# Kernel tuning notes

Hardware: AMD Instinct MI355X
Metric: run time of the kernel (lower is better)

The kernel has to match this reference:

```python
import jax, jax.numpy as jnp
import numpy as np

DIM = 2048
HEADS = 16
DIM_HEAD = 128
DIM_INNER = HEADS * DIM_HEAD  # 2048
EPS = 1.1920929e-07  # torch RMSNorm default eps = finfo(float32).eps


def setup_inputs() -> dict:
    key = jax.random.key(0)
    k_tok, k_q, k_kv, k_o = jax.random.split(key, 4)
    tokens = jax.random.normal(k_tok, (4, 2048, DIM), dtype=jnp.float32)
    # Linear weights stored as [in, out]; torch init ~ U(-1/sqrt(in), 1/sqrt(in)), use scaled normal
    s = 0.02
    w_q = jax.random.normal(k_q, (DIM, DIM_INNER), dtype=jnp.float32) * s
    w_kv = jax.random.normal(k_kv, (DIM, 2 * DIM_INNER), dtype=jnp.float32) * s
    w_out = jax.random.normal(k_o, (DIM_INNER, DIM), dtype=jnp.float32) * s
    norm_weight = jnp.ones((DIM,), dtype=jnp.float32)
    return {"tokens": tokens, "norm_weight": norm_weight, "w_q": w_q, "w_kv": w_kv, "w_out": w_out}


def _rmsnorm(x, weight):
    var = jnp.mean(jnp.square(x), axis=-1, keepdims=True)
    return x * jax.lax.rsqrt(var + EPS) * weight


def reference(tokens, norm_weight, w_q, w_kv, w_out):
    b, n, _ = tokens.shape
    x = _rmsnorm(tokens, norm_weight)
    q = x @ w_q                       # [b, n, h*d]
    kv = x @ w_kv                     # [b, n, 2*h*d]
    k, v = jnp.split(kv, 2, axis=-1)

    def split_heads(t):
        return t.reshape(b, n, HEADS, DIM_HEAD).transpose(0, 2, 1, 3)  # b h n d

    q, k, v = map(split_heads, (q, k, v))
    q = q * (DIM_HEAD ** -0.5)
    sim = jnp.einsum('bhid,bhjd->bhij', q, k)
    attn = jax.nn.softmax(sim, axis=-1)
    out = jnp.einsum('bhij,bhjd->bhid', attn, v)
    out = out.transpose(0, 2, 1, 3).reshape(b, n, DIM_INNER)
    return out @ w_out
```

## Files before the change

kernel.cpp:

```cpp
#include <hip/hip_runtime.h>
#include <hip/hip_bf16.h>
#include <stdint.h>

#define SEQ   2048
#define DIM   2048
#define HEADS 16
#define DHEAD 128
#define BATCH 4
#define MROWS (BATCH*SEQ)

typedef short bf16x8 __attribute__((ext_vector_type(8)));
typedef float f32x4  __attribute__((ext_vector_type(4)));
typedef float f32x16 __attribute__((ext_vector_type(16)));
typedef unsigned short u16x8 __attribute__((ext_vector_type(8)));
typedef unsigned int u32x4 __attribute__((ext_vector_type(4)));

__device__ __forceinline__ short f2bf(float f){
  union { float fv; unsigned u; } x; x.fv = f;
  unsigned r = x.u + 0x7fffu + ((x.u >> 16) & 1u);
  return (short)(r >> 16);
}

__device__ __forceinline__ unsigned cvtpk(float lo, float hi){
  unsigned r; asm("v_cvt_pk_bf16_f32 %0, %1, %2" : "=v"(r) : "v"(lo), "v"(hi)); return r;
}

__device__ __forceinline__ float exp2a(float x){
#if __has_builtin(__builtin_amdgcn_exp2f)
  return __builtin_amdgcn_exp2f(x);
#else
  return exp2f(x);
#endif
}

__device__ __forceinline__ void gl_lds16(const void* g, void* l){
  __builtin_amdgcn_global_load_lds((const __attribute__((address_space(1))) void*)g,
                                   (__attribute__((address_space(3))) void*)l, 16, 0, 0);
}

__device__ __forceinline__ void ofence(){
  asm volatile("" ::: "memory");
  __builtin_amdgcn_sched_barrier(0);
}

__global__ __launch_bounds__(256) void rmsnorm_cast_k(const float* __restrict__ tok,
                                                      const float* __restrict__ w,
                                                      short* __restrict__ x){
  const int row = blockIdx.x;
  const float4* r4 = (const float4*)(tok + (size_t)row * DIM);
  float4 a = r4[threadIdx.x * 2];
  float4 b = r4[threadIdx.x * 2 + 1];
  float ss = a.x*a.x + a.y*a.y + a.z*a.z + a.w*a.w
           + b.x*b.x + b.y*b.y + b.z*b.z + b.w*b.w;
  #pragma unroll
  for (int m = 1; m < 64; m <<= 1) ss += __shfl_xor(ss, m, 64);
  __shared__ float red[4];
  if ((threadIdx.x & 63) == 0) red[threadIdx.x >> 6] = ss;
  __syncthreads();
  float tot = red[0] + red[1] + red[2] + red[3];
  float rs = rsqrtf(tot * (1.0f / DIM) + 1.1920929e-07f);
  const float4* w4 = (const float4*)w;
  float4 wa = w4[threadIdx.x * 2];
  float4 wb = w4[threadIdx.x * 2 + 1];
  u16x8 o;
  o[0] = (unsigned short)f2bf(a.x * rs * wa.x);
  o[1] = (unsigned short)f2bf(a.y * rs * wa.y);
  o[2] = (unsigned short)f2bf(a.z * rs * wa.z);
  o[3] = (unsigned short)f2bf(a.w * rs * wa.w);
  o[4] = (unsigned short)f2bf(b.x * rs * wb.x);
  o[5] = (unsigned short)f2bf(b.y * rs * wb.y);
  o[6] = (unsigned short)f2bf(b.z * rs * wb.z);
  o[7] = (unsigned short)f2bf(b.w * rs * wb.w);
  *(u16x8*)(x + (size_t)row * DIM + threadIdx.x * 8) = o;
}

__global__ __launch_bounds__(256) void wtrans_k(const float* __restrict__ w,
                                                short* __restrict__ wt,
                                                int K, int N){
  __shared__ float tile[64][65];
  const int r0 = blockIdx.y * 64;
  const int c0 = blockIdx.x * 64;
  const int t = threadIdx.x;
  #pragma unroll
  for (int i = 0; i < 16; i++){
    int e = i * 256 + t; int r = e >> 6, c = e & 63;
    tile[r][c] = w[(size_t)(r0 + r) * N + c0 + c];
  }
  __syncthreads();
  #pragma unroll
  for (int i = 0; i < 16; i++){
    int e = i * 256 + t; int c = e >> 6, r = e & 63;
    wt[(size_t)(c0 + c) * K + r0 + r] = f2bf(tile[r][c]);
  }
}

__global__ __launch_bounds__(256) void vtrans_k(const short* __restrict__ kv,
                                                short* __restrict__ vt){
  __shared__ short tile[64][65];
  const int n0 = blockIdx.x * 64;
  const int d0 = blockIdx.y * 64;
  const int bh = blockIdx.z;
  const int b = bh >> 4, h = bh & 15;
  const int t = threadIdx.x;
  #pragma unroll
  for (int i = 0; i < 16; i++){
    int e = i * 256 + t; int r = e >> 6, c = e & 63;
    tile[r][c] = kv[(size_t)(b * SEQ + n0 + r) * 4096 + 2048 + h * DHEAD + d0 + c];
  }
  __syncthreads();
  #pragma unroll
  for (int i = 0; i < 16; i++){
    int e = i * 256 + t; int c = e >> 6, r = e & 63;
    vt[(size_t)(bh * DHEAD + d0 + c) * SEQ + n0 + r] = tile[r][c];
  }
}

__device__ __forceinline__ void storeC(float* C, size_t idx, float v){ C[idx] = v; }
__device__ __forceinline__ void storeC(short* C, size_t idx, float v){ C[idx] = f2bf(v); }

template<typename OutT>
__global__ __launch_bounds__(512, 2) void gemm256_k(const short* __restrict__ A,
                                                    const short* __restrict__ Bt,
                                                    OutT* __restrict__ C,
                                                    int M, int N, int K, int lgntn){
  __shared__ __align__(16) short As[4][256 * 32];
  __shared__ __align__(16) short Bs[4][256 * 32];
  const int nwg = gridDim.x;
  const int bid = blockIdx.x;
  const int o = (bid & 7) * (nwg >> 3) + (bid >> 3);
  const int bm = o >> lgntn, bn = o & ((1 << lgntn) - 1);
  const int m0 = bm << 8, n0 = bn << 8;
  const int tid = threadIdx.x, lane = tid & 63, wid = tid >> 6;
  const int l31 = lane & 31, hi = lane >> 5;
  const int wr = wid >> 2, wc = wid & 3;
  const int NT = K >> 5;

  f32x16 acc[4][2] = {};

  auto stageA = [&](int t){
    const int slot = t & 3;
    const size_t kbase = (size_t)t << 5;
    #pragma unroll
    for (int i = 0; i < 2; i++){
      int c = i * 512 + tid;
      int row = c >> 2;
      int j = (c & 3) ^ ((row >> 1) & 3);
      gl_lds16(A + (size_t)(m0 + row) * K + kbase + j * 8,
               &As[slot][(i * 512 + wid * 64) * 8]);
    }
  };
  auto stageB = [&](int t){
    const int slot = t & 3;
    const size_t kbase = (size_t)t << 5;
    #pragma unroll
    for (int i = 0; i < 2; i++){
      int c = i * 512 + tid;
      int row = c >> 2;
      int j = (c & 3) ^ ((row >> 1) & 3);
      gl_lds16(Bt + (size_t)(n0 + row) * K + kbase + j * 8,
               &Bs[slot][(i * 512 + wid * 64) * 8]);
    }
  };

  stageA(0); stageB(0); ofence();
  stageA(1); stageB(1); ofence();
  stageA(2); stageB(2); ofence();
  asm volatile("s_waitcnt vmcnt(8)" ::: "memory");
  __builtin_amdgcn_s_barrier();

  for (int t = 0; t < NT; t++){
    const short* Ab = As[t & 3];
    const short* Bb = Bs[t & 3];

    bf16x8 bfv[2][2], af0[2][2];
    #pragma unroll
    for (int nb = 0; nb < 2; nb++){
      int row = wc * 64 + nb * 32 + l31;
      #pragma unroll
      for (int ks = 0; ks < 2; ks++){
        int ch = (ks * 2 + hi) ^ ((row >> 1) & 3);
        bfv[nb][ks] = *(const bf16x8*)&Bb[row * 32 + ch * 8];
      }
    }
    #pragma unroll
    for (int mb = 0; mb < 2; mb++){
      int row = wr * 128 + mb * 32 + l31;
      #pragma unroll
      for (int ks = 0; ks < 2; ks++){
        int ch = (ks * 2 + hi) ^ ((row >> 1) & 3);
        af0[mb][ks] = *(const bf16x8*)&Ab[row * 32 + ch * 8];
      }
    }
    if (t + 3 < NT){ stageA(t + 3); ofence(); }
    __builtin_amdgcn_s_barrier();
    __builtin_amdgcn_s_setprio(1);
    #pragma unroll
    for (int mb = 0; mb < 2; mb++)
      #pragma unroll
      for (int nb = 0; nb < 2; nb++)
        #pragma unroll
        for (int ks = 0; ks < 2; ks++)
          acc[mb][nb] = __builtin_amdgcn_mfma_f32_32x32x16_bf16(af0[mb][ks], bfv[nb][ks],
                                                               acc[mb][nb], 0, 0, 0);
    __builtin_amdgcn_s_setprio(0);

    bf16x8 af1[2][2];
    #pragma unroll
    for (int mb = 0; mb < 2; mb++){
      int row = wr * 128 + (mb + 2) * 32 + l31;
      #pragma unroll
      for (int ks = 0; ks < 2; ks++){
        int ch = (ks * 2 + hi) ^ ((row >> 1) & 3);
        af1[mb][ks] = *(const bf16x8*)&Ab[row * 32 + ch * 8];
      }
    }
    if (t + 3 < NT){ stageB(t + 3); ofence(); }
    __builtin_amdgcn_s_barrier();
    __builtin_amdgcn_s_setprio(1);
    #pragma unroll
    for (int mb = 0; mb < 2; mb++)
      #pragma unroll
      for (int nb = 0; nb < 2; nb++)
        #pragma unroll
        for (int ks = 0; ks < 2; ks++)
          acc[mb + 2][nb] = __builtin_amdgcn_mfma_f32_32x32x16_bf16(af1[mb][ks], bfv[nb][ks],
                                                                   acc[mb + 2][nb], 0, 0, 0);
    __builtin_amdgcn_s_setprio(0);

    if (t + 1 < NT){
      if (t + 3 < NT)      asm volatile("s_waitcnt vmcnt(8)" ::: "memory");
      else if (t + 2 < NT) asm volatile("s_waitcnt vmcnt(4)" ::: "memory");
      else                 asm volatile("s_waitcnt vmcnt(0)" ::: "memory");
      __builtin_amdgcn_s_barrier();
    }
  }

  #pragma unroll
  for (int mb = 0; mb < 4; mb++)
    #pragma unroll
    for (int nb = 0; nb < 2; nb++)
      #pragma unroll
      for (int reg = 0; reg < 16; reg++){
        int r = (reg & 3) + 8 * (reg >> 2) + 4 * hi;
        int row = m0 + wr * 128 + mb * 32 + r;
        int col = n0 + wc * 64 + nb * 32 + l31;
        storeC(C, (size_t)row * N + col, acc[mb][nb][reg]);
      }
}

__global__ __launch_bounds__(256) void attn_k(const short* __restrict__ q,
                                              const short* __restrict__ kv,
                                              const short* __restrict__ vt,
                                              short* __restrict__ out){
  __shared__ __align__(16) short Ks[2][64 * 128];
  __shared__ __align__(16) short Vts[2][128 * 64];
  const int qt = blockIdx.x, bh = blockIdx.y;
  const int b = bh >> 4, h = bh & 15;
  const int tid = threadIdx.x, lane = tid & 63, wid = tid >> 6;
  const int l31 = lane & 31, hi = lane >> 5;
  const int qrow0 = qt * 128 + wid * 32;
  const float c2 = 0.08838834764831845f * 1.4426950408889634f;
  const int NT = SEQ / 64;

  bf16x8 qf[8];
  {
    const short* qp = q + (size_t)(b * SEQ + qrow0 + l31) * DIM + h * DHEAD + hi * 8;
    #pragma unroll
    for (int s = 0; s < 8; s++) qf[s] = *(const bf16x8*)(qp + s * 16);
  }

  f32x16 acc[4] = {};
  float m2 = -3e38f, l_s = 0.f;

  auto stage = [&](int kt, int bs){
    #pragma unroll
    for (int i = 0; i < 4; i++){
      int cb = (i * 4 + wid) * 64;
      int c  = cb + lane;
      int kr = c >> 4, kj = (c & 15) ^ (kr & 7);
      gl_lds16(kv + (size_t)(b * SEQ + kt * 64 + kr) * 4096 + h * DHEAD + kj * 8,
               &Ks[bs][cb * 8]);
      int vr = c >> 3, vj = (c & 7) ^ (vr & 7);
      gl_lds16(vt + (size_t)(bh * DHEAD + vr) * SEQ + kt * 64 + vj * 8,
               &Vts[bs][cb * 8]);
    }
  };

  stage(0, 0);
  int cur = 0;

  for (int kt = 0; kt < NT; kt++){
    if (kt + 1 < NT){
      stage(kt + 1, cur ^ 1);
      asm volatile("s_waitcnt vmcnt(8)" ::: "memory");
    } else {
      asm volatile("s_waitcnt vmcnt(0)" ::: "memory");
    }
    __builtin_amdgcn_s_barrier();

    const short* Kb = Ks[cur];
    const short* Vb = Vts[cur];

    f32x16 t0 = {0,0,0,0,0,0,0,0,0,0,0,0,0,0,0,0};
    f32x16 t1 = t0;
    {
      const int r0 = l31, r1 = l31 + 32;
      #pragma unroll
      for (int s = 0; s < 8; s++){
        bf16x8 k0 = *(const bf16x8*)&Kb[r0 * 128 + (((2 * s + hi) ^ (r0 & 7)) * 8)];
        bf16x8 k1 = *(const bf16x8*)&Kb[r1 * 128 + (((2 * s + hi) ^ (r1 & 7)) * 8)];
        t0 = __builtin_amdgcn_mfma_f32_32x32x16_bf16(k0, qf[s], t0, 0, 0, 0);
        t1 = __builtin_amdgcn_mfma_f32_32x32x16_bf16(k1, qf[s], t1, 0, 0, 0);
      }
    }

    float mxr = t0[0];
    #pragma unroll
    for (int i = 1; i < 16; i++) mxr = fmaxf(mxr, t0[i]);
    #pragma unroll
    for (int i = 0; i < 16; i++) mxr = fmaxf(mxr, t1[i]);
    mxr = fmaxf(mxr, __shfl_xor(mxr, 32));
    float mx2 = mxr * c2;
    if (!__all(mx2 <= m2 + 11.5f)){
      float m2n = fmaxf(m2, mx2);
      float al = exp2a(m2 - m2n);
      m2 = m2n;
      l_s *= al;
      #pragma unroll
      for (int reg = 0; reg < 16; reg++){
        float ar = __shfl(al, (reg & 3) + 8 * (reg >> 2) + 4 * hi);
        #pragma unroll
        for (int dt = 0; dt < 4; dt++) acc[dt][reg] *= ar;
      }
    }

    float ps = 0.f;
    unsigned w[16];
    #pragma unroll
    for (int pr = 0; pr < 8; pr++){
      float pa_ = exp2a(fmaf(t0[2 * pr], c2, -m2));
      float pb_ = exp2a(fmaf(t0[2 * pr + 1], c2, -m2));
      ps += pa_ + pb_;
      w[pr] = cvtpk(pa_, pb_);
    }
    #pragma unroll
    for (int pr = 0; pr < 8; pr++){
      float pa_ = exp2a(fmaf(t1[2 * pr], c2, -m2));
      float pb_ = exp2a(fmaf(t1[2 * pr + 1], c2, -m2));
      ps += pa_ + pb_;
      w[8 + pr] = cvtpk(pa_, pb_);
    }
    ps += __shfl_xor(ps, 32);
    l_s += ps;

    #pragma unroll
    for (int fp = 0; fp < 4; fp++){
      unsigned A0 = w[fp * 4 + 0], A1 = w[fp * 4 + 1];
      unsigned B0 = w[fp * 4 + 2], B1 = w[fp * 4 + 3];
      unsigned xA0 = __shfl_xor((int)A0, 32), xA1 = __shfl_xor((int)A1, 32);
      unsigned xB0 = __shfl_xor((int)B0, 32), xB1 = __shfl_xor((int)B1, 32);
      u32x4 fw;
      fw[0] = hi ? xB0 : A0;
      fw[1] = hi ? xB1 : A1;
      fw[2] = hi ? B0 : xA0;
      fw[3] = hi ? B1 : xA1;
      union { u32x4 u; bf16x8 v; } pc; pc.u = fw;
      #pragma unroll
      for (int dt = 0; dt < 4; dt++){
        int vr = dt * 32 + l31;
        bf16x8 vb = *(const bf16x8*)&Vb[vr * 64 + (((2 * fp + hi) ^ (vr & 7)) * 8)];
        acc[dt] = __builtin_amdgcn_mfma_f32_32x32x16_bf16(pc.v, vb, acc[dt], 0, 0, 0);
      }
    }

    asm volatile("s_waitcnt lgkmcnt(0)" ::: "memory");
    __builtin_amdgcn_s_barrier();
    cur ^= 1;
  }

  float inv = 1.0f / l_s;
  #pragma unroll
  for (int reg = 0; reg < 16; reg++){
    int cr = (reg & 3) + 8 * (reg >> 2) + 4 * hi;
    float li = __shfl(inv, cr);
    int row = qrow0 + cr;
    #pragma unroll
    for (int dt = 0; dt < 4; dt++)
      out[(size_t)(b * SEQ + row) * DIM + h * DHEAD + dt * 32 + l31] = f2bf(acc[dt][reg] * li);
  }
}

extern "C" void kernel_launch(void* const* d_in, const int* in_sizes, int n_in,
                              void* d_out, int out_size, void* d_ws, size_t ws_size,
                              hipStream_t stream) {
  (void)in_sizes; (void)n_in; (void)out_size; (void)ws_size;
  const float* tokens = (const float*)d_in[0];
  const float* normw  = (const float*)d_in[1];
  const float* wq     = (const float*)d_in[2];
  const float* wkv    = (const float*)d_in[3];
  const float* wout   = (const float*)d_in[4];
  float* outp = (float*)d_out;
  char* ws = (char*)d_ws;

  short* x     = (short*)(ws + 0);
  short* wqt   = (short*)(ws + 33554432);
  short* wkvt  = (short*)(ws + 41943040);
  short* woutt = (short*)(ws + 58720256);
  short* qb    = (short*)(ws + 67108864);
  short* kvb   = (short*)(ws + 100663296);
  short* vtb   = (short*)(ws + 167772160);

  rmsnorm_cast_k<<<dim3(MROWS), dim3(256), 0, stream>>>(tokens, normw, x);
  wtrans_k<<<dim3(2048/64, 2048/64), dim3(256), 0, stream>>>(wq,   wqt,   2048, 2048);
  wtrans_k<<<dim3(4096/64, 2048/64), dim3(256), 0, stream>>>(wkv,  wkvt,  2048, 4096);
  wtrans_k<<<dim3(2048/64, 2048/64), dim3(256), 0, stream>>>(wout, woutt, 2048, 2048);
  gemm256_k<short><<<dim3((MROWS/256)*(2048/256)), dim3(512), 0, stream>>>(x, wqt,  qb,  MROWS, 2048, 2048, 3);
  gemm256_k<short><<<dim3((MROWS/256)*(4096/256)), dim3(512), 0, stream>>>(x, wkvt, kvb, MROWS, 4096, 2048, 4);
  vtrans_k<<<dim3(SEQ/64, DHEAD/64, BATCH*HEADS), dim3(256), 0, stream>>>(kvb, vtb);
  attn_k<<<dim3(SEQ/128, BATCH*HEADS), dim3(256), 0, stream>>>(qb, kvb, vtb, qb);
  gemm256_k<float><<<dim3((MROWS/256)*(2048/256)), dim3(512), 0, stream>>>(qb, woutt, outp, MROWS, 2048, 2048, 3);
}
```

Before: 589.6 us.

## Interleave per-half softmax with PV MFMAs, widen K swizzle, add setprio

The attention loop now processes each 32-key half on its own: it computes the online-softmax max and exp for one half, then immediately issues that half's PV MFMAs before starting the second half. The aim is to overlap exp and VALU work with matrix-core work. The K tile's LDS XOR swizzle widens from 8 to 16 chunks to cut bank conflicts on K reads, and the max reduction becomes a tree. s_setprio is raised around the MFMA blocks. In exchange, the rescale check and cross-lane shuffles now run twice per tile.

```diff
diff --git a/kernel.cpp b/kernel.cpp
--- a/kernel.cpp
+++ b/kernel.cpp
@@ -277,7 +277,7 @@
     for (int i = 0; i < 4; i++){
       int cb = (i * 4 + wid) * 64;
       int c  = cb + lane;
-      int kr = c >> 4, kj = (c & 15) ^ (kr & 7);
+      int kr = c >> 4, kj = (c & 15) ^ (kr & 15);
       gl_lds16(kv + (size_t)(b * SEQ + kt * 64 + kr) * 4096 + h * DHEAD + kj * 8,
                &Ks[bs][cb * 8]);
       int vr = c >> 3, vj = (c & 7) ^ (vr & 7);
@@ -286,40 +286,15 @@
     }
   };
 
-  stage(0, 0);
-  int cur = 0;
-
-  for (int kt = 0; kt < NT; kt++){
-    if (kt + 1 < NT){
-      stage(kt + 1, cur ^ 1);
-      asm volatile("s_waitcnt vmcnt(8)" ::: "memory");
-    } else {
-      asm volatile("s_waitcnt vmcnt(0)" ::: "memory");
-    }
-    __builtin_amdgcn_s_barrier();
-
-    const short* Kb = Ks[cur];
-    const short* Vb = Vts[cur];
-
-    f32x16 t0 = {0,0,0,0,0,0,0,0,0,0,0,0,0,0,0,0};
-    f32x16 t1 = t0;
-    {
-      const int r0 = l31, r1 = l31 + 32;
-      #pragma unroll
-      for (int s = 0; s < 8; s++){
-        bf16x8 k0 = *(const bf16x8*)&Kb[r0 * 128 + (((2 * s + hi) ^ (r0 & 7)) * 8)];
-        bf16x8 k1 = *(const bf16x8*)&Kb[r1 * 128 + (((2 * s + hi) ^ (r1 & 7)) * 8)];
-        t0 = __builtin_amdgcn_mfma_f32_32x32x16_bf16(k0, qf[s], t0, 0, 0, 0);
-        t1 = __builtin_amdgcn_mfma_f32_32x32x16_bf16(k1, qf[s], t1, 0, 0, 0);
-      }
-    }
-
-    float mxr = t0[0];
-    #pragma unroll
-    for (int i = 1; i < 16; i++) mxr = fmaxf(mxr, t0[i]);
-    #pragma unroll
-    for (int i = 0; i < 16; i++) mxr = fmaxf(mxr, t1[i]);
-    mxr = fmaxf(mxr, __shfl_xor(mxr, 32));
+  auto smpack = [&](f32x16& t, unsigned* wv){
+    float mr[8];
+    #pragma unroll
+    for (int i = 0; i < 8; i++) mr[i] = fmaxf(t[i], t[i + 8]);
+    #pragma unroll
+    for (int s = 4; s > 0; s >>= 1)
+      #pragma unroll
+      for (int i = 0; i < s; i++) mr[i] = fmaxf(mr[i], mr[i + s]);
+    float mxr = fmaxf(mr[0], __shfl_xor(mr[0], 32));
     float mx2 = mxr * c2;
     if (!__all(mx2 <= m2 + 11.5f)){
       float m2n = fmaxf(m2, mx2);
@@ -333,30 +308,24 @@
         for (int dt = 0; dt < 4; dt++) acc[dt][reg] *= ar;
       }
     }
-
-    float ps = 0.f;
-    unsigned w[16];
+    float p0 = 0.f, p1 = 0.f;
     #pragma unroll
     for (int pr = 0; pr < 8; pr++){
-      float pa_ = exp2a(fmaf(t0[2 * pr], c2, -m2));
-      float pb_ = exp2a(fmaf(t0[2 * pr + 1], c2, -m2));
-      ps += pa_ + pb_;
-      w[pr] = cvtpk(pa_, pb_);
-    }
-    #pragma unroll
-    for (int pr = 0; pr < 8; pr++){
-      float pa_ = exp2a(fmaf(t1[2 * pr], c2, -m2));
-      float pb_ = exp2a(fmaf(t1[2 * pr + 1], c2, -m2));
-      ps += pa_ + pb_;
-      w[8 + pr] = cvtpk(pa_, pb_);
-    }
+      float pa_ = exp2a(fmaf(t[2 * pr], c2, -m2));
+      float pb_ = exp2a(fmaf(t[2 * pr + 1], c2, -m2));
+      p0 += pa_; p1 += pb_;
+      wv[pr] = cvtpk(pa_, pb_);
+    }
+    float ps = p0 + p1;
     ps += __shfl_xor(ps, 32);
     l_s += ps;
-
-    #pragma unroll
-    for (int fp = 0; fp < 4; fp++){
-      unsigned A0 = w[fp * 4 + 0], A1 = w[fp * 4 + 1];
-      unsigned B0 = w[fp * 4 + 2], B1 = w[fp * 4 + 3];
+  };
+
+  auto pv = [&](const short* Vb, int sub, const unsigned* wv){
+    #pragma unroll
+    for (int fpl = 0; fpl < 2; fpl++){
+      unsigned A0 = wv[fpl * 4 + 0], A1 = wv[fpl * 4 + 1];
+      unsigned B0 = wv[fpl * 4 + 2], B1 = wv[fpl * 4 + 3];
       unsigned xA0 = __shfl_xor((int)A0, 32), xA1 = __shfl_xor((int)A1, 32);
       unsigned xB0 = __shfl_xor((int)B0, 32), xB1 = __shfl_xor((int)B1, 32);
       u32x4 fw;
@@ -365,13 +334,55 @@
       fw[2] = hi ? B0 : xA0;
       fw[3] = hi ? B1 : xA1;
       union { u32x4 u; bf16x8 v; } pc; pc.u = fw;
+      const int fp = sub * 2 + fpl;
+      __builtin_amdgcn_s_setprio(1);
       #pragma unroll
       for (int dt = 0; dt < 4; dt++){
         int vr = dt * 32 + l31;
         bf16x8 vb = *(const bf16x8*)&Vb[vr * 64 + (((2 * fp + hi) ^ (vr & 7)) * 8)];
         acc[dt] = __builtin_amdgcn_mfma_f32_32x32x16_bf16(pc.v, vb, acc[dt], 0, 0, 0);
       }
-    }
+      __builtin_amdgcn_s_setprio(0);
+    }
+  };
+
+  stage(0, 0);
+  int cur = 0;
+
+  for (int kt = 0; kt < NT; kt++){
+    if (kt + 1 < NT){
+      stage(kt + 1, cur ^ 1);
+      asm volatile("s_waitcnt vmcnt(8)" ::: "memory");
+    } else {
+      asm volatile("s_waitcnt vmcnt(0)" ::: "memory");
+    }
+    __builtin_amdgcn_s_barrier();
+
+    const short* Kb = Ks[cur];
+    const short* Vb = Vts[cur];
+
+    f32x16 t0 = {0,0,0,0,0,0,0,0,0,0,0,0,0,0,0,0};
+    f32x16 t1 = t0;
+    {
+      const int r0 = l31, r1 = l31 + 32;
+      const int rs4 = l31 & 15;
+      __builtin_amdgcn_s_setprio(1);
+      #pragma unroll
+      for (int s = 0; s < 8; s++){
+        int ch = (2 * s + hi) ^ rs4;
+        bf16x8 k0 = *(const bf16x8*)&Kb[r0 * 128 + ch * 8];
+        bf16x8 k1 = *(const bf16x8*)&Kb[r1 * 128 + ch * 8];
+        t0 = __builtin_amdgcn_mfma_f32_32x32x16_bf16(k0, qf[s], t0, 0, 0, 0);
+        t1 = __builtin_amdgcn_mfma_f32_32x32x16_bf16(k1, qf[s], t1, 0, 0, 0);
+      }
+      __builtin_amdgcn_s_setprio(0);
+    }
+
+    unsigned w0[8], w1[8];
+    smpack(t0, w0);
+    pv(Vb, 0, w0);
+    smpack(t1, w1);
+    pv(Vb, 1, w1);
 
     asm volatile("s_waitcnt lgkmcnt(0)" ::: "memory");
     __builtin_amdgcn_s_barrier();
```

Result: slower. 650.7 us (+10.4%).
